# Optimization experiments

Measured on AMD Instinct MI355X. Metric: run time of the kernel, lower is better.

The kernel has to match this reference:

```python
import jax, jax.numpy as jnp
import numpy as np

ARITY = 8        # children per node (< max_child_number=10, so all children used)
TREE_DEPTH = 5   # internal levels 1..5; depth=5 so GRU applies at every internal node
DIM = 384        # cgf_input_dim == GRU input == GRU hidden (unidirectional, n_layers=1)
VOCAB = 32000


def gru_seq(xs, h0, w_ih, w_hh, b_ih, b_hh):
    # xs: [S, N, D] sequence-major, h0: [N, D]. torch nn.GRU gate order: r, z, n.
    def step(h, x_t):
        gi = x_t @ w_ih.T + b_ih            # [N, 3D]
        gh = h @ w_hh.T + b_hh              # [N, 3D]
        i_r, i_z, i_n = jnp.split(gi, 3, axis=-1)
        h_r, h_z, h_n = jnp.split(gh, 3, axis=-1)
        r = jax.nn.sigmoid(i_r + h_r)
        z = jax.nn.sigmoid(i_z + h_z)
        n = jnp.tanh(i_n + r * h_n)
        h_new = (1.0 - z) * n + z * h
        return h_new, h_new
    h_last, outs = jax.lax.scan(step, h0, xs)
    return outs, h_last                      # [S, N, D], [N, D]


def setup_inputs() -> dict:
    key = jax.random.key(0)
    k1, k2, k3, k4, k5, k6 = jax.random.split(key, 6)
    n_leaves = ARITY ** TREE_DEPTH
    s = 1.0 / np.sqrt(DIM)
    return {
        "leaf_tokens": jax.random.randint(k1, (n_leaves,), 0, VOCAB, dtype=jnp.int32),
        "embed_table": jax.random.normal(k2, (VOCAB, DIM), jnp.float32),
        "w_ih": jax.random.uniform(k3, (3 * DIM, DIM), jnp.float32, -s, s),
        "w_hh": jax.random.uniform(k4, (3 * DIM, DIM), jnp.float32, -s, s),
        "b_ih": jax.random.uniform(k5, (3 * DIM,), jnp.float32, -s, s),
        "b_hh": jax.random.uniform(k6, (3 * DIM,), jnp.float32, -s, s),
    }


def reference(leaf_tokens, embed_table, w_ih, w_hh, b_ih, b_hh):
    # Leaves: embedding-dict lookup -> x=[1,1,D] per leaf; h = zeros.
    x = embed_table[leaf_tokens]             # [A^T, D]
    h = jnp.zeros_like(x)                    # leaf hidden states are zeros
    # Level-synchronous post-order: process deepest internal level first.
    for level in range(TREE_DEPTH, 0, -1):
        n_parents = ARITY ** (level - 1)
        # Children are consumed from last to first (loop i = len-1 .. 0), so
        # the GRU sequence is the REVERSED child order.
        xs = x.reshape(n_parents, ARITY, DIM)[:, ::-1, :].transpose(1, 0, 2)  # [A, P, D]
        h0 = h.reshape(n_parents, ARITY, DIM).mean(axis=1)                     # mean of child hiddens
        outs, h = gru_seq(xs, h0, w_ih, w_hh, b_ih, b_hh)
        x = outs.mean(axis=0)                # mean over the child sequence -> node output [P, D]
    # Root (layer=1) returns res = out of shape [1,1,D]
    return x.reshape(1, 1, DIM)
```

## Files before the change

kernel.cpp:

```cpp
#include <hip/hip_runtime.h>
#include <hip/hip_bf16.h>
#include <stdint.h>

typedef float f32x4 __attribute__((ext_vector_type(4)));
typedef short bf16x8 __attribute__((ext_vector_type(8)));

#define NSLOT 21
#define NDS 24
#define NCTR 1033
#define CI(i) ((i) * 32)

__device__ __forceinline__ ushort to_bf16(float f) {
    union { float f; uint32_t u; } v; v.f = f;
    uint32_t u = v.u;
    return (ushort)((u + 0x7fffu + ((u >> 16) & 1u)) >> 16);
}
__device__ __forceinline__ float sigmoid_(float x) { return 1.0f / (1.0f + __expf(-x)); }
__device__ __forceinline__ float tanh_(float x)    { return 1.0f - 2.0f / (__expf(2.0f * x) + 1.0f); }

__device__ __forceinline__ void st_sc1_u16(ushort* p, ushort v) {
    asm volatile("global_store_short %0, %1, off sc1" :: "v"(p), "v"((uint32_t)v) : "memory");
}
__device__ __forceinline__ void st_sc1_f32(float* p, float v) {
    asm volatile("global_store_dword %0, %1, off sc1" :: "v"(p), "v"(v) : "memory");
}

__global__ void prep_w(const float* __restrict__ w_ih, const float* __restrict__ w_hh,
                       ushort* __restrict__ wswz, unsigned int* __restrict__ ctr) {
    int tid = blockIdx.x * blockDim.x + threadIdx.x;
    if (tid < NCTR * 32) ctr[tid] = 0u;
    if (tid >= 1152 * 96) return;
    int g  = tid / 96;
    int k  = (tid % 96) * 8;
    int kc = k >> 5;
    int q  = (k >> 3) & 3;
    int tile = g >> 4;
    int lane = q * 16 + (g & 15);
    ushort* dst = wswz + ((size_t)(tile * 24 + kc) * 64 + lane) * 8;
    const float* src = (k < 384) ? (w_ih + (size_t)g * 384 + k)
                                 : (w_hh + (size_t)g * 384 + (k - 384));
#pragma unroll
    for (int j = 0; j < 8; ++j) dst[j] = to_bf16(src[j]);
}

__global__ void embed_gather(const int* __restrict__ tok, const float* __restrict__ table,
                             ushort* __restrict__ xleaf, int n_leaves) {
    int tid = blockIdx.x * blockDim.x + threadIdx.x;
    if (tid >= n_leaves * 48) return;
    int leaf = tid / 48, i = tid % 48;
    const float* src = table + (size_t)tok[leaf] * 384 + i * 8;
    bf16x8 v;
#pragma unroll
    for (int j = 0; j < 8; ++j) v[j] = (short)to_bf16(src[j]);
    *(bf16x8*)(xleaf + (size_t)leaf * 384 + i * 8) = v;
}

__device__ __forceinline__ void wait_ge(unsigned int* c, unsigned int n) {
    while (true) {
        for (int k = 0; k < 64; ++k) {
            if (__hip_atomic_load(c, __ATOMIC_RELAXED, __HIP_MEMORY_SCOPE_AGENT) >= n) return;
            __builtin_amdgcn_s_sleep(2);
        }
        if (__hip_atomic_load(c, __ATOMIC_ACQUIRE, __HIP_MEMORY_SCOPE_AGENT) >= n) return;
    }
}

__device__ __forceinline__ void sync_group(unsigned int* c) {
    __syncthreads();
    if (threadIdx.x == 0) {
        __hip_atomic_fetch_add(c, 1u, __ATOMIC_RELEASE, __HIP_MEMORY_SCOPE_AGENT);
        wait_ge(c, NDS);
    }
    __syncthreads();
}

__device__ __forceinline__ void full_barrier(unsigned int* grpSlot, unsigned int* master) {
    __syncthreads();
    if (threadIdx.x == 0) {
        unsigned int old = __hip_atomic_fetch_add(grpSlot, 1u, __ATOMIC_RELEASE, __HIP_MEMORY_SCOPE_AGENT);
        if (old == NDS - 1)
            __hip_atomic_fetch_add(master, 1u, __ATOMIC_RELEASE, __HIP_MEMORY_SCOPE_AGENT);
        wait_ge(master, NSLOT);
    }
    __syncthreads();
}

__global__ __launch_bounds__(256, 2)
void tree_gru(const ushort* __restrict__ XA, const ushort* __restrict__ W,
              const float* __restrict__ b_ih, const float* __restrict__ b_hh,
              ushort* __restrict__ HBar, float* __restrict__ Hfar,
              ushort* __restrict__ Xoar,
              unsigned int* __restrict__ ctr, float* __restrict__ out)
{
    __shared__ __align__(16) ushort lw[36864];
    const int slot = blockIdx.x, ds = blockIdx.y;
    const int tid = threadIdx.x;
    const int wave = tid >> 6, lane = tid & 63;
    const int quad = lane >> 4, col = lane & 15;
    const int d = ds * 16 + col;

    {
        bf16x8* dstv = (bf16x8*)lw;
#pragma unroll
        for (int g = 0; g < 3; ++g) {
            const bf16x8* s = (const bf16x8*)(W + (size_t)(g * NDS + ds) * 12288);
#pragma unroll
            for (int i = 0; i < 6; ++i) dstv[g * 1536 + i * 256 + tid] = s[i * 256 + tid];
        }
    }
    __syncthreads();

    const float br = b_ih[d] + b_hh[d];
    const float bz = b_ih[384 + d] + b_hh[384 + d];
    const float bi = b_ih[768 + d], bh = b_hh[768 + d];
    const ushort* lwr = &lw[(size_t)lane * 8];

#pragma unroll 1
    for (int lvl = 0; lvl < 5; ++lvl) {
        const int P  = (lvl == 0) ? 4096 : (lvl == 1) ? 512 : (lvl == 2) ? 64 : (lvl == 3) ? 8 : 1;
        const int rp = (lvl == 0) ? 0 : (lvl == 1) ? 4096 : (lvl == 2) ? 4608 : (lvl == 3) ? 4672 : 4680;
        const int rpPrev = (lvl == 1) ? 0 : (lvl == 2) ? 4096 : (lvl == 3) ? 4608 : 4672;
        const int nmp = (P + 31) >> 5;
        const bool leaf = (lvl == 0), root = (lvl == 4);
        const ushort* Xc   = leaf ? XA : (Xoar + (size_t)384 * rpPrev);
        const float* Hfprev = leaf ? nullptr : (Hfar + (size_t)384 * rpPrev);
        ushort* HBlvl = HBar + (size_t)9 * 384 * rp;
        ushort* Xout  = Xoar + (size_t)384 * rp;
        float*  Hfout = root ? nullptr : (Hfar + (size_t)384 * rp);
        const size_t N = (size_t)P * 384;
        const bool act = (slot * 4 < nmp);
        if (act) {
            const int  mpA = slot * 4 + wave;
            const int  mpB = mpA + NSLOT * 4;
            const bool hasA = mpA < nmp;
            const bool hasB = mpB < nmp;
            float hpA[2][4], hsA[2][4], hpB[2][4], hsB[2][4];
#pragma unroll
            for (int mt = 0; mt < 2; ++mt)
#pragma unroll
                for (int r = 0; r < 4; ++r) {
                    hsA[mt][r] = 0.f; hsB[mt][r] = 0.f;
                    hpA[mt][r] = 0.f; hpB[mt][r] = 0.f;
                }
            if (!leaf) {
                auto prol = [&](int mp, float (&hp)[2][4]) {
                    const int m0 = mp * 32;
#pragma unroll
                    for (int mt = 0; mt < 2; ++mt)
#pragma unroll
                        for (int r = 0; r < 4; ++r) {
                            const int m = m0 + mt * 16 + quad * 4 + r;
                            if (m < P) {
                                const float* hc = Hfprev + (size_t)m * 8 * 384 + d;
                                float h0 = 0.f;
#pragma unroll
                                for (int c = 0; c < 8; ++c) h0 += hc[(size_t)c * 384];
                                h0 *= 0.125f;
                                hp[mt][r] = h0;
                                st_sc1_u16(&HBlvl[(size_t)m * 384 + d], to_bf16(h0));
                            }
                        }
                };
                if (hasA) prol(mpA, hpA);
                if (hasB) prol(mpB, hpB);
                sync_group(&ctr[CI((lvl * 9 + 8) * NSLOT + slot)]);
            }
#pragma unroll 1
            for (int t = 0; t < 8; ++t) {
                const ushort* HBp = HBlvl + (size_t)t * N;
                ushort*       HBn = HBlvl + (size_t)(t + 1) * N;
                const bool hz   = leaf && (t == 0);
                const bool last = (t == 7);
                const int  child = 7 - t;
                auto stepf = [&](int mp, float (&hp)[2][4], float (&hs)[2][4]) {
                    const int m0 = mp * 32;
                    const bool do2 = (m0 + 16) < P;
                    const int par0 = m0 + col, par1 = m0 + 16 + col;
                    const bool av0 = par0 < P, av1 = par1 < P;
                    const ushort* xr0 = Xc + ((size_t)par0 * 8 + child) * 384 + quad * 8;
                    const ushort* xr1 = Xc + ((size_t)par1 * 8 + child) * 384 + quad * 8;
                    const ushort* hr0 = HBp + (size_t)par0 * 384 + quad * 8;
                    const ushort* hr1 = HBp + (size_t)par1 * 384 + quad * 8;
                    const f32x4 z4 = (f32x4){0.f, 0.f, 0.f, 0.f};
                    f32x4 accr0 = z4, accz0 = z4, accn10 = z4, accn20 = z4;
                    f32x4 accr1 = z4, accz1 = z4, accn11 = z4, accn21 = z4;
                    const bf16x8 zf = (bf16x8){0, 0, 0, 0, 0, 0, 0, 0};
#pragma unroll
                    for (int kc = 0; kc < 12; ++kc) {
                        bf16x8 a0 = zf, a1 = zf;
                        if (av0) a0 = *(const bf16x8*)(xr0 + kc * 32);
                        if (do2 && av1) a1 = *(const bf16x8*)(xr1 + kc * 32);
                        bf16x8 bR = *(const bf16x8*)(lwr + kc * 512);
                        bf16x8 bZ = *(const bf16x8*)(lwr + 12288 + kc * 512);
                        bf16x8 bN = *(const bf16x8*)(lwr + 24576 + kc * 512);
                        accr0  = __builtin_amdgcn_mfma_f32_16x16x32_bf16(a0, bR, accr0, 0, 0, 0);
                        accz0  = __builtin_amdgcn_mfma_f32_16x16x32_bf16(a0, bZ, accz0, 0, 0, 0);
                        accn10 = __builtin_amdgcn_mfma_f32_16x16x32_bf16(a0, bN, accn10, 0, 0, 0);
                        if (do2) {
                            accr1  = __builtin_amdgcn_mfma_f32_16x16x32_bf16(a1, bR, accr1, 0, 0, 0);
                            accz1  = __builtin_amdgcn_mfma_f32_16x16x32_bf16(a1, bZ, accz1, 0, 0, 0);
                            accn11 = __builtin_amdgcn_mfma_f32_16x16x32_bf16(a1, bN, accn11, 0, 0, 0);
                        }
                    }
                    if (!hz) {
#pragma unroll
                        for (int kc = 0; kc < 12; ++kc) {
                            bf16x8 a0 = zf, a1 = zf;
                            if (av0) a0 = *(const bf16x8*)(hr0 + kc * 32);
                            if (do2 && av1) a1 = *(const bf16x8*)(hr1 + kc * 32);
                            bf16x8 bR = *(const bf16x8*)(lwr + (12 + kc) * 512);
                            bf16x8 bZ = *(const bf16x8*)(lwr + 12288 + (12 + kc) * 512);
                            bf16x8 bN = *(const bf16x8*)(lwr + 24576 + (12 + kc) * 512);
                            accr0  = __builtin_amdgcn_mfma_f32_16x16x32_bf16(a0, bR, accr0, 0, 0, 0);
                            accz0  = __builtin_amdgcn_mfma_f32_16x16x32_bf16(a0, bZ, accz0, 0, 0, 0);
                            accn20 = __builtin_amdgcn_mfma_f32_16x16x32_bf16(a0, bN, accn20, 0, 0, 0);
                            if (do2) {
                                accr1  = __builtin_amdgcn_mfma_f32_16x16x32_bf16(a1, bR, accr1, 0, 0, 0);
                                accz1  = __builtin_amdgcn_mfma_f32_16x16x32_bf16(a1, bZ, accz1, 0, 0, 0);
                                accn21 = __builtin_amdgcn_mfma_f32_16x16x32_bf16(a1, bN, accn21, 0, 0, 0);
                            }
                        }
                    }
#pragma unroll
                    for (int mt = 0; mt < 2; ++mt) {
                        if (mt && !do2) break;
                        const f32x4 ar  = mt ? accr1  : accr0;
                        const f32x4 az  = mt ? accz1  : accz0;
                        const f32x4 an1 = mt ? accn11 : accn10;
                        const f32x4 an2 = mt ? accn21 : accn20;
#pragma unroll
                        for (int r = 0; r < 4; ++r) {
                            const int m = m0 + mt * 16 + quad * 4 + r;
                            if (m < P) {
                                const size_t idx = (size_t)m * 384 + d;
                                float rv = sigmoid_(ar[r] + br);
                                float zv = sigmoid_(az[r] + bz);
                                float nv = tanh_(an1[r] + bi + rv * (an2[r] + bh));
                                float hn = (1.0f - zv) * nv + zv * hp[mt][r];
                                hp[mt][r] = hn;
                                hs[mt][r] += hn;
                                if (!last) {
                                    st_sc1_u16(&HBn[idx], to_bf16(hn));
                                } else {
                                    float xo = hs[mt][r] * 0.125f;
                                    st_sc1_u16(&Xout[idx], to_bf16(xo));
                                    if (!root) st_sc1_f32(&Hfout[idx], hn);
                                    else if (m == 0) out[d] = xo;
                                }
                            }
                        }
                    }
                };
                if (hasA) stepf(mpA, hpA, hsA);
                if (hasB) stepf(mpB, hpB, hsB);
                if (t < 7) sync_group(&ctr[CI((lvl * 9 + t) * NSLOT + slot)]);
            }
        }
        if (lvl < 4) full_barrier(&ctr[CI(945 + lvl * NSLOT + slot)], &ctr[CI(1029 + lvl)]);
    }
}

extern "C" void kernel_launch(void* const* d_in, const int* in_sizes, int n_in,
                              void* d_out, int out_size, void* d_ws, size_t ws_size,
                              hipStream_t stream) {
    const int*   tok   = (const int*)d_in[0];
    const float* table = (const float*)d_in[1];
    const float* w_ih  = (const float*)d_in[2];
    const float* w_hh  = (const float*)d_in[3];
    const float* b_ih  = (const float*)d_in[4];
    const float* b_hh  = (const float*)d_in[5];
    float* out = (float*)d_out;

    char* ws = (char*)d_ws;
    size_t off = 0;
    auto alloc = [&](size_t bytes) -> void* {
        void* p = ws + off;
        off = (off + bytes + 255) & ~(size_t)255;
        return p;
    };
    ushort* wswz = (ushort*)alloc((size_t)1152 * 768 * 2);
    ushort* XA   = (ushort*)alloc((size_t)32768 * 384 * 2);
    ushort* HBar = (ushort*)alloc((size_t)9 * 4681 * 384 * 2);
    float*  Hfar = (float*)alloc((size_t)4680 * 384 * 4);
    ushort* Xoar = (ushort*)alloc((size_t)4681 * 384 * 2);
    unsigned int* ctr = (unsigned int*)alloc((size_t)NCTR * 32 * 4);

    prep_w<<<(1152 * 96 + 255) / 256, 256, 0, stream>>>(w_ih, w_hh, wswz, ctr);
    embed_gather<<<(32768 * 48 + 255) / 256, 256, 0, stream>>>(tok, table, XA, 32768);
    tree_gru<<<dim3(NSLOT, NDS), 256, 0, stream>>>(XA, wswz, b_ih, b_hh,
                                                   HBar, Hfar, Xoar, ctr, out);
}
```

Measured before the change: 726.5 us.

## Overlap input-projection MFMAs with group barrier wait and vectorize hidden stores

Splits each GRU step into an input part (x @ W_ih) and a hidden part (h @ W_hh). The input projection for the next child is computed between arriving at and waiting on the inter-block group barrier, so barrier latency is hidden behind independent MFMA work. Hidden-state writes are staged through LDS and issued as 128-bit stores instead of scattered 16-bit stores. The spin-wait also polls more often with system scope. Costs are extra accumulator registers held across the barrier and a small amount of extra LDS.

Result: no change. 723.4 us (-0.4%).

```diff
diff --git a/kernel.cpp b/kernel.cpp
--- a/kernel.cpp
+++ b/kernel.cpp
@@ -23,6 +23,9 @@
 }
 __device__ __forceinline__ void st_sc1_f32(float* p, float v) {
     asm volatile("global_store_dword %0, %1, off sc1" :: "v"(p), "v"(v) : "memory");
+}
+__device__ __forceinline__ void st_sc1_b128(void* p, bf16x8 v) {
+    asm volatile("global_store_dwordx4 %0, %1, off sc1" :: "v"(p), "v"(v) : "memory");
 }
 
 __global__ void prep_w(const float* __restrict__ w_ih, const float* __restrict__ w_hh,
@@ -57,20 +60,21 @@
 
 __device__ __forceinline__ void wait_ge(unsigned int* c, unsigned int n) {
     while (true) {
-        for (int k = 0; k < 64; ++k) {
-            if (__hip_atomic_load(c, __ATOMIC_RELAXED, __HIP_MEMORY_SCOPE_AGENT) >= n) return;
-            __builtin_amdgcn_s_sleep(2);
+        for (int k = 0; k < 512; ++k) {
+            if (__hip_atomic_load(c, __ATOMIC_RELAXED, __HIP_MEMORY_SCOPE_SYSTEM) >= n) return;
+            __builtin_amdgcn_s_sleep(1);
         }
         if (__hip_atomic_load(c, __ATOMIC_ACQUIRE, __HIP_MEMORY_SCOPE_AGENT) >= n) return;
     }
 }
 
-__device__ __forceinline__ void sync_group(unsigned int* c) {
-    __syncthreads();
-    if (threadIdx.x == 0) {
+__device__ __forceinline__ void group_arrive(unsigned int* c) {
+    __syncthreads();
+    if (threadIdx.x == 0)
         __hip_atomic_fetch_add(c, 1u, __ATOMIC_RELEASE, __HIP_MEMORY_SCOPE_AGENT);
-        wait_ge(c, NDS);
-    }
+}
+__device__ __forceinline__ void group_wait(unsigned int* c) {
+    if (threadIdx.x == 0) wait_ge(c, NDS);
     __syncthreads();
 }
 
@@ -93,6 +97,7 @@
               unsigned int* __restrict__ ctr, float* __restrict__ out)
 {
     __shared__ __align__(16) ushort lw[36864];
+    __shared__ __align__(16) ushort stage[4][512];
     const int slot = blockIdx.x, ds = blockIdx.y;
     const int tid = threadIdx.x;
     const int wave = tid >> 6, lane = tid & 63;
@@ -122,7 +127,7 @@
         const int rpPrev = (lvl == 1) ? 0 : (lvl == 2) ? 4096 : (lvl == 3) ? 4608 : 4672;
         const int nmp = (P + 31) >> 5;
         const bool leaf = (lvl == 0), root = (lvl == 4);
-        const ushort* Xc   = leaf ? XA : (Xoar + (size_t)384 * rpPrev);
+        const ushort* Xc = leaf ? XA : (Xoar + (size_t)384 * rpPrev);
         const float* Hfprev = leaf ? nullptr : (Hfar + (size_t)384 * rpPrev);
         ushort* HBlvl = HBar + (size_t)9 * 384 * rp;
         ushort* Xout  = Xoar + (size_t)384 * rp;
@@ -130,8 +135,8 @@
         const size_t N = (size_t)P * 384;
         const bool act = (slot * 4 < nmp);
         if (act) {
-            const int  mpA = slot * 4 + wave;
-            const int  mpB = mpA + NSLOT * 4;
+            const int mpA = slot * 4 + wave;
+            const int mpB = mpA + NSLOT * 4;
             const bool hasA = mpA < nmp;
             const bool hasB = mpB < nmp;
             float hpA[2][4], hsA[2][4], hpB[2][4], hsB[2][4];
@@ -139,31 +144,133 @@
             for (int mt = 0; mt < 2; ++mt)
 #pragma unroll
                 for (int r = 0; r < 4; ++r) {
-                    hsA[mt][r] = 0.f; hsB[mt][r] = 0.f;
-                    hpA[mt][r] = 0.f; hpB[mt][r] = 0.f;
-                }
-            if (!leaf) {
-                auto prol = [&](int mp, float (&hp)[2][4]) {
-                    const int m0 = mp * 32;
-#pragma unroll
-                    for (int mt = 0; mt < 2; ++mt)
-#pragma unroll
-                        for (int r = 0; r < 4; ++r) {
-                            const int m = m0 + mt * 16 + quad * 4 + r;
-                            if (m < P) {
-                                const float* hc = Hfprev + (size_t)m * 8 * 384 + d;
-                                float h0 = 0.f;
-#pragma unroll
-                                for (int c = 0; c < 8; ++c) h0 += hc[(size_t)c * 384];
-                                h0 *= 0.125f;
-                                hp[mt][r] = h0;
-                                st_sc1_u16(&HBlvl[(size_t)m * 384 + d], to_bf16(h0));
+                    hpA[mt][r] = 0.f; hsA[mt][r] = 0.f;
+                    hpB[mt][r] = 0.f; hsB[mt][r] = 0.f;
+                }
+            const f32x4 z4 = (f32x4){0.f, 0.f, 0.f, 0.f};
+            const bf16x8 zf = (bf16x8){0, 0, 0, 0, 0, 0, 0, 0};
+            struct XA6 { f32x4 r[2], z[2], n[2]; } xA, xB;
+
+            auto xpart = [&](int mp, int child, XA6& o) {
+                const int m0 = mp * 32;
+                const bool do2 = (m0 + 16) < P;
+                const int par0 = m0 + col, par1 = m0 + 16 + col;
+                const bool av0 = par0 < P, av1 = par1 < P;
+                const ushort* xr0 = Xc + ((size_t)par0 * 8 + child) * 384 + quad * 8;
+                const ushort* xr1 = Xc + ((size_t)par1 * 8 + child) * 384 + quad * 8;
+                o.r[0] = z4; o.z[0] = z4; o.n[0] = z4;
+                o.r[1] = z4; o.z[1] = z4; o.n[1] = z4;
+#pragma unroll
+                for (int kc = 0; kc < 12; ++kc) {
+                    bf16x8 a0 = zf, a1 = zf;
+                    if (av0) a0 = *(const bf16x8*)(xr0 + kc * 32);
+                    if (do2 && av1) a1 = *(const bf16x8*)(xr1 + kc * 32);
+                    bf16x8 bR = *(const bf16x8*)(lwr + kc * 512);
+                    bf16x8 bZ = *(const bf16x8*)(lwr + 12288 + kc * 512);
+                    bf16x8 bN = *(const bf16x8*)(lwr + 24576 + kc * 512);
+                    o.r[0] = __builtin_amdgcn_mfma_f32_16x16x32_bf16(a0, bR, o.r[0], 0, 0, 0);
+                    o.z[0] = __builtin_amdgcn_mfma_f32_16x16x32_bf16(a0, bZ, o.z[0], 0, 0, 0);
+                    o.n[0] = __builtin_amdgcn_mfma_f32_16x16x32_bf16(a0, bN, o.n[0], 0, 0, 0);
+                    if (do2) {
+                        o.r[1] = __builtin_amdgcn_mfma_f32_16x16x32_bf16(a1, bR, o.r[1], 0, 0, 0);
+                        o.z[1] = __builtin_amdgcn_mfma_f32_16x16x32_bf16(a1, bZ, o.z[1], 0, 0, 0);
+                        o.n[1] = __builtin_amdgcn_mfma_f32_16x16x32_bf16(a1, bN, o.n[1], 0, 0, 0);
+                    }
+                }
+            };
+            auto prol = [&](int mp, float (&hp)[2][4]) {
+                const int m0 = mp * 32;
+#pragma unroll
+                for (int mt = 0; mt < 2; ++mt)
+#pragma unroll
+                    for (int r = 0; r < 4; ++r) {
+                        const int m = m0 + mt * 16 + quad * 4 + r;
+                        if (m < P) {
+                            const float* hc = Hfprev + (size_t)m * 8 * 384 + d;
+                            float h0 = 0.f;
+#pragma unroll
+                            for (int c = 0; c < 8; ++c) h0 += hc[(size_t)c * 384];
+                            h0 *= 0.125f;
+                            hp[mt][r] = h0;
+                            st_sc1_u16(&HBlvl[(size_t)m * 384 + d], to_bf16(h0));
+                        }
+                    }
+            };
+            auto hpart = [&](int mp, XA6& x, float (&hp)[2][4], float (&hs)[2][4],
+                             const ushort* HBp, ushort* HBn, bool hz, bool last) {
+                const int m0 = mp * 32;
+                const bool do2 = (m0 + 16) < P;
+                const int par0 = m0 + col, par1 = m0 + 16 + col;
+                const bool av0 = par0 < P, av1 = par1 < P;
+                f32x4 n2a = z4, n2b = z4;
+                if (!hz) {
+                    const ushort* hr0 = HBp + (size_t)par0 * 384 + quad * 8;
+                    const ushort* hr1 = HBp + (size_t)par1 * 384 + quad * 8;
+#pragma unroll
+                    for (int kc = 0; kc < 12; ++kc) {
+                        bf16x8 a0 = zf, a1 = zf;
+                        if (av0) a0 = *(const bf16x8*)(hr0 + kc * 32);
+                        if (do2 && av1) a1 = *(const bf16x8*)(hr1 + kc * 32);
+                        bf16x8 bR = *(const bf16x8*)(lwr + (12 + kc) * 512);
+                        bf16x8 bZ = *(const bf16x8*)(lwr + 12288 + (12 + kc) * 512);
+                        bf16x8 bN = *(const bf16x8*)(lwr + 24576 + (12 + kc) * 512);
+                        x.r[0] = __builtin_amdgcn_mfma_f32_16x16x32_bf16(a0, bR, x.r[0], 0, 0, 0);
+                        x.z[0] = __builtin_amdgcn_mfma_f32_16x16x32_bf16(a0, bZ, x.z[0], 0, 0, 0);
+                        n2a    = __builtin_amdgcn_mfma_f32_16x16x32_bf16(a0, bN, n2a, 0, 0, 0);
+                        if (do2) {
+                            x.r[1] = __builtin_amdgcn_mfma_f32_16x16x32_bf16(a1, bR, x.r[1], 0, 0, 0);
+                            x.z[1] = __builtin_amdgcn_mfma_f32_16x16x32_bf16(a1, bZ, x.z[1], 0, 0, 0);
+                            n2b    = __builtin_amdgcn_mfma_f32_16x16x32_bf16(a1, bN, n2b, 0, 0, 0);
+                        }
+                    }
+                }
+#pragma unroll
+                for (int mt = 0; mt < 2; ++mt) {
+                    if (mt && !do2) break;
+                    const f32x4 ar = x.r[mt], az = x.z[mt], an1 = x.n[mt];
+                    const f32x4 an2 = mt ? n2b : n2a;
+#pragma unroll
+                    for (int r = 0; r < 4; ++r) {
+                        const int m = m0 + mt * 16 + quad * 4 + r;
+                        if (m < P) {
+                            float rv = sigmoid_(ar[r] + br);
+                            float zv = sigmoid_(az[r] + bz);
+                            float nv = tanh_(an1[r] + bi + rv * (an2[r] + bh));
+                            float hn = (1.0f - zv) * nv + zv * hp[mt][r];
+                            hp[mt][r] = hn;
+                            hs[mt][r] += hn;
+                            if (last) {
+                                const size_t idx = (size_t)m * 384 + d;
+                                float xo = hs[mt][r] * 0.125f;
+                                st_sc1_u16(&Xout[idx], to_bf16(xo));
+                                if (!root) st_sc1_f32(&Hfout[idx], hn);
+                                else if (m == 0) out[d] = xo;
+                            } else {
+                                stage[wave][(mt * 16 + quad * 4 + r) * 16 + col] = to_bf16(hn);
                             }
                         }
-                };
+                    }
+                }
+                if (!last) {
+                    const int row = lane >> 1, half = lane & 1;
+                    const int m = m0 + row;
+                    if (m < P) {
+                        bf16x8 v = *(const bf16x8*)&stage[wave][row * 16 + half * 8];
+                        st_sc1_b128(HBn + (size_t)m * 384 + ds * 16 + half * 8, v);
+                    }
+                }
+            };
+
+            if (!leaf) {
                 if (hasA) prol(mpA, hpA);
                 if (hasB) prol(mpB, hpB);
-                sync_group(&ctr[CI((lvl * 9 + 8) * NSLOT + slot)]);
+                group_arrive(&ctr[CI((lvl * 9 + 8) * NSLOT + slot)]);
+                if (hasA) xpart(mpA, 7, xA);
+                if (hasB) xpart(mpB, 7, xB);
+                group_wait(&ctr[CI((lvl * 9 + 8) * NSLOT + slot)]);
+            } else {
+                if (hasA) xpart(mpA, 7, xA);
+                if (hasB) xpart(mpB, 7, xB);
             }
 #pragma unroll 1
             for (int t = 0; t < 8; ++t) {
@@ -171,89 +278,16 @@
                 ushort*       HBn = HBlvl + (size_t)(t + 1) * N;
                 const bool hz   = leaf && (t == 0);
                 const bool last = (t == 7);
-                const int  child = 7 - t;
-                auto stepf = [&](int mp, float (&hp)[2][4], float (&hs)[2][4]) {
-                    const int m0 = mp * 32;
-                    const bool do2 = (m0 + 16) < P;
-                    const int par0 = m0 + col, par1 = m0 + 16 + col;
-                    const bool av0 = par0 < P, av1 = par1 < P;
-                    const ushort* xr0 = Xc + ((size_t)par0 * 8 + child) * 384 + quad * 8;
-                    const ushort* xr1 = Xc + ((size_t)par1 * 8 + child) * 384 + quad * 8;
-                    const ushort* hr0 = HBp + (size_t)par0 * 384 + quad * 8;
-                    const ushort* hr1 = HBp + (size_t)par1 * 384 + quad * 8;
-                    const f32x4 z4 = (f32x4){0.f, 0.f, 0.f, 0.f};
-                    f32x4 accr0 = z4, accz0 = z4, accn10 = z4, accn20 = z4;
-                    f32x4 accr1 = z4, accz1 = z4, accn11 = z4, accn21 = z4;
-                    const bf16x8 zf = (bf16x8){0, 0, 0, 0, 0, 0, 0, 0};
-#pragma unroll
-                    for (int kc = 0; kc < 12; ++kc) {
-                        bf16x8 a0 = zf, a1 = zf;
-                        if (av0) a0 = *(const bf16x8*)(xr0 + kc * 32);
-                        if (do2 && av1) a1 = *(const bf16x8*)(xr1 + kc * 32);
-                        bf16x8 bR = *(const bf16x8*)(lwr + kc * 512);
-                        bf16x8 bZ = *(const bf16x8*)(lwr + 12288 + kc * 512);
-                        bf16x8 bN = *(const bf16x8*)(lwr + 24576 + kc * 512);
-                        accr0  = __builtin_amdgcn_mfma_f32_16x16x32_bf16(a0, bR, accr0, 0, 0, 0);
-                        accz0  = __builtin_amdgcn_mfma_f32_16x16x32_bf16(a0, bZ, accz0, 0, 0, 0);
-                        accn10 = __builtin_amdgcn_mfma_f32_16x16x32_bf16(a0, bN, accn10, 0, 0, 0);
-                        if (do2) {
-                            accr1  = __builtin_amdgcn_mfma_f32_16x16x32_bf16(a1, bR, accr1, 0, 0, 0);
-                            accz1  = __builtin_amdgcn_mfma_f32_16x16x32_bf16(a1, bZ, accz1, 0, 0, 0);
-                            accn11 = __builtin_amdgcn_mfma_f32_16x16x32_bf16(a1, bN, accn11, 0, 0, 0);
-                        }
-                    }
-                    if (!hz) {
-#pragma unroll
-                        for (int kc = 0; kc < 12; ++kc) {
-                            bf16x8 a0 = zf, a1 = zf;
-                            if (av0) a0 = *(const bf16x8*)(hr0 + kc * 32);
-                            if (do2 && av1) a1 = *(const bf16x8*)(hr1 + kc * 32);
-                            bf16x8 bR = *(const bf16x8*)(lwr + (12 + kc) * 512);
-                            bf16x8 bZ = *(const bf16x8*)(lwr + 12288 + (12 + kc) * 512);
-                            bf16x8 bN = *(const bf16x8*)(lwr + 24576 + (12 + kc) * 512);
-                            accr0  = __builtin_amdgcn_mfma_f32_16x16x32_bf16(a0, bR, accr0, 0, 0, 0);
-                            accz0  = __builtin_amdgcn_mfma_f32_16x16x32_bf16(a0, bZ, accz0, 0, 0, 0);
-                            accn20 = __builtin_amdgcn_mfma_f32_16x16x32_bf16(a0, bN, accn20, 0, 0, 0);
-                            if (do2) {
-                                accr1  = __builtin_amdgcn_mfma_f32_16x16x32_bf16(a1, bR, accr1, 0, 0, 0);
-                                accz1  = __builtin_amdgcn_mfma_f32_16x16x32_bf16(a1, bZ, accz1, 0, 0, 0);
-                                accn21 = __builtin_amdgcn_mfma_f32_16x16x32_bf16(a1, bN, accn21, 0, 0, 0);
-                            }
-                        }
-                    }
-#pragma unroll
-                    for (int mt = 0; mt < 2; ++mt) {
-                        if (mt && !do2) break;
-                        const f32x4 ar  = mt ? accr1  : accr0;
-                        const f32x4 az  = mt ? accz1  : accz0;
-                        const f32x4 an1 = mt ? accn11 : accn10;
-                        const f32x4 an2 = mt ? accn21 : accn20;
-#pragma unroll
-                        for (int r = 0; r < 4; ++r) {
-                            const int m = m0 + mt * 16 + quad * 4 + r;
-                            if (m < P) {
-                                const size_t idx = (size_t)m * 384 + d;
-                                float rv = sigmoid_(ar[r] + br);
-                                float zv = sigmoid_(az[r] + bz);
-                                float nv = tanh_(an1[r] + bi + rv * (an2[r] + bh));
-                                float hn = (1.0f - zv) * nv + zv * hp[mt][r];
-                                hp[mt][r] = hn;
-                                hs[mt][r] += hn;
-                                if (!last) {
-                                    st_sc1_u16(&HBn[idx], to_bf16(hn));
-                                } else {
-                                    float xo = hs[mt][r] * 0.125f;
-                                    st_sc1_u16(&Xout[idx], to_bf16(xo));
-                                    if (!root) st_sc1_f32(&Hfout[idx], hn);
-                                    else if (m == 0) out[d] = xo;
-                                }
-                            }
-                        }
-                    }
-                };
-                if (hasA) stepf(mpA, hpA, hsA);
-                if (hasB) stepf(mpB, hpB, hsB);
-                if (t < 7) sync_group(&ctr[CI((lvl * 9 + t) * NSLOT + slot)]);
+                if (hasA) hpart(mpA, xA, hpA, hsA, HBp, HBn, hz, last);
+                if (hasB) hpart(mpB, xB, hpB, hsB, HBp, HBn, hz, last);
+                if (!last) {
+                    unsigned int* c = &ctr[CI((lvl * 9 + t) * NSLOT + slot)];
+                    group_arrive(c);
+                    const int nchild = 6 - t;
+                    if (hasA) xpart(mpA, nchild, xA);
+                    if (hasB) xpart(mpB, nchild, xB);
+                    group_wait(c);
+                }
             }
         }
         if (lvl < 4) full_barrier(&ctr[CI(945 + lvl * NSLOT + slot)], &ctr[CI(1029 + lvl)]);
```
